# Performance work log

Hardware: AMD Instinct MI355X
Metric: run time of the kernel (lower is better)

The kernel has to match this reference:

```python
import jax, jax.numpy as jnp
import numpy as np

# --- static forest structure: NT complete ternary trees of depth DEPTH ---
BR, DEPTH, NT = 3, 7, 64            # branching factor (=L), edge-levels, num trees
OFF = [(3 ** d - 1) // 2 for d in range(DEPTH + 2)]  # BFS level offsets within a tree
NPT = OFF[DEPTH + 1]                 # nodes per tree = 3280
DIM = NT * NPT                       # total nodes = 209920
C_DIM, NGEN, M_SYM = 8, 8, 128


def build_tree():
    """Returns pos, leaves, batch, roots, levels [(parent_idx, child_idx)], unique-parents per level."""
    base = (np.arange(NT) * NPT)[:, None]
    pos = np.zeros(DIM, dtype=np.int64)
    levels, upar = [], []
    for d in range(1, DEPTH + 1):
        loc = np.arange(OFF[d], OFF[d + 1])
        ch = (base + loc).ravel()                                 # children at depth d (tree-major)
        pa = (base + (OFF[d - 1] + (loc - OFF[d]) // BR)).ravel() # their parents
        pos[ch] = np.tile((loc - OFF[d]) % BR, NT)
        levels.append((pa, ch))
        upar.append((base + np.arange(OFF[d - 1], OFF[d])).ravel())  # unique parents of level d
    leaves = (base + np.arange(OFF[DEPTH], OFF[DEPTH + 1])).ravel()
    batch = np.repeat(np.arange(NT), NPT)
    roots = np.arange(NT) * NPT
    return pos, leaves, batch, roots, levels, upar


def setup_inputs() -> dict:
    key = jax.random.key(0)
    k1, k2, k3, k4, k5 = jax.random.split(key, 5)
    pos_np, leaves_np, batch_np, _, _, _ = build_tree()
    return {
        "lam_A": jax.random.uniform(k1, (C_DIM, C_DIM, BR, NGEN), dtype=jnp.float32),
        "lam_B": jax.random.uniform(k2, (C_DIM, M_SYM, NGEN), dtype=jnp.float32),
        "lam_Pi": jax.random.uniform(k3, (C_DIM, BR, NGEN), dtype=jnp.float32),
        "lam_SP": jax.random.uniform(k4, (BR, NGEN), dtype=jnp.float32),
        "x": jax.random.randint(k5, (DIM,), 0, M_SYM, dtype=jnp.int64),
        "pos": jnp.asarray(pos_np),
        "leaves": jnp.asarray(leaves_np),
        "batch": jnp.asarray(batch_np),
    }


def reference(lam_A, lam_B, lam_Pi, lam_SP, x, pos, leaves, batch):
    # ReversedUpwardDownward (mode='bu') of PosteriorHiddenTreeMarkovModel.
    A = jax.nn.softmax(lam_A, axis=0)   # (C,C,L,G): softmax over first state axis
    Bm = jax.nn.softmax(lam_B, axis=1)  # (C,M,G): softmax over symbols
    Pi = jax.nn.softmax(lam_Pi, axis=0) # (C,L,G)
    SP = jax.nn.softmax(lam_SP, axis=0) # (L,G)
    C, G = A.shape[0], A.shape[-1]
    _, _, _, roots, levels, upar = build_tree()  # static structure

    beta = jnp.zeros((DIM, C, G), lam_A.dtype)
    t_beta = jnp.zeros((DIM, C, G), lam_A.dtype)

    # --- leaves init ---
    Pi_leaves = Pi[:, pos[leaves]]            # (C,Nl,G)
    bl = jnp.transpose(Pi_leaves * Bm[:, x[leaves]], (1, 0, 2))  # (Nl,C,G)
    beta = beta.at[leaves].set(bl / bl.sum(1, keepdims=True))

    # --- upward pass (deepest level first) ---
    for (pa, ch), u in zip(reversed(levels), reversed(upar)):
        SP_ch = SP[pos[ch]][:, None, None, :]                 # (E,1,1,G)
        A_ch = jnp.transpose(A[:, :, pos[ch]], (2, 0, 1, 3))  # (E,C,C,G)
        tb = (SP_ch * A_ch * beta[ch][:, None]).sum(2)        # (E,C,G) sum over child state
        t_beta = t_beta.at[pa].add(tb)
        bu = t_beta[u] * jnp.transpose(Bm[:, x[u]], (1, 0, 2))
        beta = beta.at[u].set(bu / bu.sum(1, keepdims=True))

    # --- downward pass ---
    eps = jnp.zeros((DIM, C, G), lam_A.dtype)
    ell = jnp.zeros((DIM, G), lam_A.dtype)
    eps = eps.at[roots].set(beta[roots])
    for pa, ch in levels:
        SP_ch = SP[pos[ch]]                                   # (E,G)
        A_ch = jnp.transpose(A[:, :, pos[ch]], (2, 0, 1, 3))  # (E,C,C,G)
        trans = SP_ch[:, None, None, :] * A_ch
        ej = (eps[pa][:, :, None, :] * trans * beta[ch][:, None, :, :]
              / t_beta[pa][:, :, None, :])                    # (E,C,C,G) joint posterior
        eps = eps.at[ch].set(ej.sum(1))
        ell = ell.at[ch].add((ej * jnp.log(A_ch)).sum((1, 2))
                             + ej.sum((1, 2)) * jnp.log(SP_ch))
    ell = ell + (eps * jnp.transpose(Bm[:, x], (1, 0, 2))).sum(1)
    ell = ell.at[leaves].add((eps[leaves] * jnp.transpose(jnp.log(Pi_leaves), (1, 0, 2))).sum(1))
    return -jax.ops.segment_sum(ell, batch, num_segments=NT)  # (NT,G)
```

## Files before the change

### kernel.cpp

```cpp
#include <hip/hip_runtime.h>
#include <hip/hip_fp16.h>


namespace {

constexpr int kNPT = 3280;
constexpr int kRS  = 72;
constexpr int kAS  = 68;
constexpr unsigned kMAGIC  = 0x13579BDFu;
constexpr unsigned kMAGIC2 = 0x2468ACEFu;
__device__ __constant__ int LO[6] = {0, 1, 4, 13, 40, 121};
__device__ __constant__ int P3[5] = {1, 3, 9, 27, 81};

#define AGENT_LD(p)    __hip_atomic_load((p), __ATOMIC_RELAXED, __HIP_MEMORY_SCOPE_AGENT)
#define AGENT_ST(p, v) __hip_atomic_store((p), (v), __ATOMIC_RELAXED, __HIP_MEMORY_SCOPE_AGENT)

__device__ __forceinline__ void leaf_beta(const float* __restrict__ sPi,
                                          const float* __restrict__ pBm,
                                          int p, int xv, int g, float* b)
{
    float s = 0.f;
    #pragma unroll
    for (int c = 0; c < 8; ++c) {
        b[c] = sPi[(c * 3 + p) * 8 + g] * pBm[xv * 64 + c * 8 + g];
        s += b[c];
    }
    float ig = __builtin_amdgcn_rcpf(s);
    #pragma unroll
    for (int c = 0; c < 8; ++c) b[c] *= ig;
}

__device__ __forceinline__ void matvec_acc(const float* __restrict__ arow,
                                           const float* __restrict__ bj,
                                           float spg, float* acc)
{
    #pragma unroll
    for (int j = 0; j < 8; ++j) {
        float4 a0 = *(const float4*)(arow + j * 8);
        float4 a1 = *(const float4*)(arow + j * 8 + 4);
        float cjv = spg * bj[j];
        acc[0] = fmaf(a0.x, cjv, acc[0]); acc[1] = fmaf(a0.y, cjv, acc[1]);
        acc[2] = fmaf(a0.z, cjv, acc[2]); acc[3] = fmaf(a0.w, cjv, acc[3]);
        acc[4] = fmaf(a1.x, cjv, acc[4]); acc[5] = fmaf(a1.y, cjv, acc[5]);
        acc[6] = fmaf(a1.z, cjv, acc[6]); acc[7] = fmaf(a1.w, cjv, acc[7]);
    }
}

__global__ __launch_bounds__(256, 2)
void fused(const float* __restrict__ lamA, const float* __restrict__ lamB,
           const float* __restrict__ lamPi, const float* __restrict__ lamSP,
           const int* __restrict__ x, float* __restrict__ out,
           unsigned* __restrict__ sy, float* __restrict__ bmG,
           float* __restrict__ b3, float* __restrict__ e3)
{
    const int tid = threadIdx.x, w = tid >> 6, lane = tid & 63;
    const int n = lane >> 3, g = lane & 7;
    __shared__ __align__(16) float sAg[24 * kAS];
    __shared__ __align__(16) float sLAg[24 * kAS];
    __shared__ float sPi[192], sLPi[192], sSP[24], sLSP[24];
    __shared__ float bW[4][40 * kRS];
    __shared__ __half bMidH[13 * 64];
    __shared__ float sMs[13 * 8];
    __shared__ unsigned char xW[4][124];
    unsigned* trCnt = sy + 32;
    unsigned* trFlg = sy + 2080;

    if (tid == 0) {
        if (blockIdx.x == 0) {
            for (int i = 0; i < 64; ++i) AGENT_ST(&trCnt[i * 32], 0u);
            __builtin_amdgcn_s_waitcnt(0);
            AGENT_ST(&sy[0], kMAGIC);
        }
        unsigned long sp = 0;
        while (AGENT_LD(&sy[0]) != kMAGIC) {
            if (++sp > (1UL << 24)) break;
            __builtin_amdgcn_s_sleep(2);
        }
    }
    __syncthreads();

    if (blockIdx.x == 0) {
        float* rr = &bW[0][0];
        int row = tid >> 2, part = tid & 3;
        int c = row >> 3, gg = row & 7, m0 = part * 32;
        float mx = -1e30f;
        for (int mm = 0; mm < 32; ++mm)
            mx = fmaxf(mx, lamB[(c * 128 + m0 + mm) * 8 + gg]);
        rr[tid] = mx;
        __syncthreads();
        float m4 = fmaxf(fmaxf(rr[row * 4], rr[row * 4 + 1]),
                         fmaxf(rr[row * 4 + 2], rr[row * 4 + 3]));
        float s = 0.f;
        for (int mm = 0; mm < 32; ++mm)
            s += expf(lamB[(c * 128 + m0 + mm) * 8 + gg] - m4);
        rr[256 + tid] = s;
        __syncthreads();
        float stot = rr[256 + row * 4] + rr[256 + row * 4 + 1]
                   + rr[256 + row * 4 + 2] + rr[256 + row * 4 + 3];
        float inv = 1.f / stot;
        for (int mm = 0; mm < 32; ++mm)
            AGENT_ST(&bmG[(m0 + mm) * 64 + c * 8 + gg],
                     expf(lamB[(c * 128 + m0 + mm) * 8 + gg] - m4) * inv);
        __syncthreads();
        if (tid == 0) AGENT_ST(&sy[4], kMAGIC2);
    }
    for (int col = tid; col < 192; col += 256) {
        int j = col / 24; int rem = col - j * 24; int p = rem >> 3; int gg = rem & 7;
        float v[8]; float mx = -1e30f;
        #pragma unroll
        for (int i = 0; i < 8; ++i) {
            v[i] = lamA[((i * 8 + j) * 3 + p) * 8 + gg];
            mx = fmaxf(mx, v[i]);
        }
        float s = 0.f;
        #pragma unroll
        for (int i = 0; i < 8; ++i) { v[i] = expf(v[i] - mx); s += v[i]; }
        float inv = 1.f / s;
        int base = (gg * 3 + p) * kAS + j * 8;
        #pragma unroll
        for (int i = 0; i < 8; ++i) {
            float sm = v[i] * inv;
            sAg[base + i]  = sm;
            sLAg[base + i] = sm * logf(sm);
        }
    }
    for (int col = tid; col < 24; col += 256) {
        int p = col >> 3; int gg = col & 7;
        float v[8]; float mx = -1e30f;
        #pragma unroll
        for (int c = 0; c < 8; ++c) {
            v[c] = lamPi[(c * 3 + p) * 8 + gg];
            mx = fmaxf(mx, v[c]);
        }
        float s = 0.f;
        #pragma unroll
        for (int c = 0; c < 8; ++c) { v[c] = expf(v[c] - mx); s += v[c]; }
        float inv = 1.f / s;
        #pragma unroll
        for (int c = 0; c < 8; ++c) {
            int idx = (c * 3 + p) * 8 + gg;
            float sm = v[c] * inv;
            sPi[idx]  = sm;
            sLPi[idx] = logf(sm);
        }
    }
    if (tid < 8) {
        int gg = tid;
        float v0 = lamSP[gg], v1 = lamSP[8 + gg], v2 = lamSP[16 + gg];
        float mx = fmaxf(v0, fmaxf(v1, v2));
        float e0 = expf(v0 - mx), e1 = expf(v1 - mx), e2 = expf(v2 - mx);
        float inv = 1.f / (e0 + e1 + e2);
        sSP[gg] = e0 * inv; sSP[8 + gg] = e1 * inv; sSP[16 + gg] = e2 * inv;
        sLSP[gg] = logf(e0 * inv); sLSP[8 + gg] = logf(e1 * inv); sLSP[16 + gg] = logf(e2 * inv);
    }
    if (tid == 0) {
        unsigned long sp = 0;
        while (AGENT_LD(&sy[4]) != kMAGIC2) {
            if (++sp > (1UL << 24)) break;
            __builtin_amdgcn_s_sleep(2);
        }
        __threadfence();
    }
    __syncthreads();

    const float* pBm = bmG;
    const int id = blockIdx.x * 4 + w, t = id / 27, q = id % 27, xb = t * kNPT;
    float* bw = &bW[w][0];
    unsigned char* xw = &xW[w][0];

    for (int u = lane; u < 121; u += 64) {
        int gx;
        if (u == 0)       gx = 13 + q;
        else if (u < 4)   gx = 40  + q * 3  + (u - 1);
        else if (u < 13)  gx = 121 + q * 9  + (u - 4);
        else if (u < 40)  gx = 364 + q * 27 + (u - 13);
        else              gx = 1093 + q * 81 + (u - 40);
        xw[u] = (unsigned char)x[xb + gx];
    }
    __builtin_amdgcn_wave_barrier();

    for (int e = 3; e >= 0; --e) {
        int cnt = P3[e];
        for (int base = 0; base < cnt; base += 8) {
            int node = base + n;
            if (node < cnt) {
                float acc[8];
                #pragma unroll
                for (int i = 0; i < 8; ++i) acc[i] = 0.f;
                #pragma unroll
                for (int k = 0; k < 3; ++k) {
                    float bj[8];
                    if (e == 3) {
                        leaf_beta(sPi, pBm, k, xw[40 + 3 * node + k], g, bj);
                    } else {
                        int co = (LO[e + 1] + 3 * node + k) * kRS + g;
                        #pragma unroll
                        for (int j = 0; j < 8; ++j) bj[j] = bw[co + j * 8];
                    }
                    matvec_acc(&sAg[(g * 3 + k) * kAS], bj, sSP[k * 8 + g], acc);
                }
                if (e == 0) {
                    #pragma unroll
                    for (int i = 0; i < 8; ++i) bw[i * 8 + g] = acc[i];
                    int xv = xw[0];
                    float s = 0.f;
                    #pragma unroll
                    for (int i = 0; i < 8; ++i) { acc[i] *= pBm[xv * 64 + i * 8 + g]; s += acc[i]; }
                    float ig = __builtin_amdgcn_rcpf(s);
                    #pragma unroll
                    for (int i = 0; i < 8; ++i)
                        AGENT_ST(&b3[id * 64 + i * 8 + g], acc[i] * ig);
                } else {
                    int slot = LO[e] + node;
                    int xv = xw[slot];
                    float s = 0.f;
                    #pragma unroll
                    for (int i = 0; i < 8; ++i) { acc[i] *= pBm[xv * 64 + i * 8 + g]; s += acc[i]; }
                    float ig = __builtin_amdgcn_rcpf(s);
                    int bo = slot * kRS + g;
                    #pragma unroll
                    for (int i = 0; i < 8; ++i) bw[bo + i * 8] = acc[i] * ig;
                    bw[slot * kRS + 64 + g] = s;
                }
            }
        }
        __builtin_amdgcn_wave_barrier();
    }
    __builtin_amdgcn_s_waitcnt(0);
    if (lane == 0)
        __hip_atomic_fetch_add(&trCnt[t * 32], 1u, __ATOMIC_RELAXED,
                               __HIP_MEMORY_SCOPE_AGENT);

    if (q == 0) {
        unsigned long sp = 0;
        while (AGENT_LD(&trCnt[t * 32]) < 27u) {
            if (++sp > (1UL << 22)) break;
            __builtin_amdgcn_s_sleep(1);
        }
        __threadfence();
        float ellm = 0.f;
        for (int f = 2; f >= 0; --f) {
            int cnt = (f == 2) ? 9 : (f == 1 ? 3 : 1);
            int pl0 = (f == 2) ? 4 : (f == 1 ? 1 : 0);
            int cl0 = (f == 1) ? 4 : 1;
            for (int base = 0; base < cnt; base += 8) {
                int pi = base + n;
                if (pi < cnt) {
                    float acc[8];
                    #pragma unroll
                    for (int i = 0; i < 8; ++i) acc[i] = 0.f;
                    #pragma unroll
                    for (int k = 0; k < 3; ++k) {
                        float bj[8];
                        if (f == 2) {
                            const float* src = b3 + (t * 27 + 3 * pi + k) * 64 + g;
                            #pragma unroll
                            for (int j = 0; j < 8; ++j) bj[j] = src[j * 8];
                        } else {
                            int co = (cl0 + 3 * pi + k) * 64 + g;
                            #pragma unroll
                            for (int j = 0; j < 8; ++j)
                                bj[j] = __half2float(bMidH[co + j * 8]);
                        }
                        matvec_acc(&sAg[(g * 3 + k) * kAS], bj, sSP[k * 8 + g], acc);
                    }
                    int slot = pl0 + pi;
                    int xv = x[xb + slot];
                    float s = 0.f;
                    #pragma unroll
                    for (int i = 0; i < 8; ++i) { acc[i] *= pBm[xv * 64 + i * 8 + g]; s += acc[i]; }
                    float ig = __builtin_amdgcn_rcpf(s);
                    int bo = slot * 64 + g;
                    #pragma unroll
                    for (int i = 0; i < 8; ++i)
                        bMidH[bo + i * 8] = __float2half(acc[i] * ig);
                    sMs[slot * 8 + g] = s;
                }
            }
            __builtin_amdgcn_wave_barrier();
        }
        if (n == 0) {
            int xv = x[xb];
            float invs = __builtin_amdgcn_rcpf(sMs[g]);
            #pragma unroll
            for (int c = 0; c < 8; ++c)
                ellm += __half2float(bMidH[c * 8 + g]) * pBm[xv * 64 + c * 8 + g];
            #pragma unroll
            for (int c = 0; c < 8; ++c)
                bMidH[c * 8 + g] = __float2half(pBm[xv * 64 + c * 8 + g] * invs);
        }
        __builtin_amdgcn_wave_barrier();
        for (int f = 1; f <= 3; ++f) {
            int cnt = (f == 1) ? 3 : (f == 2 ? 9 : 27);
            int cl0 = (f == 1) ? 1 : (f == 2 ? 4 : 13);
            int pl0 = (f == 1) ? 0 : (f == 2 ? 1 : 4);
            for (int base = 0; base < cnt; base += 8) {
                int ci = base + n;
                if (ci < cnt) {
                    int p = ci % 3;
                    int ps = (pl0 + ci / 3) * 64 + g;
                    float r[8];
                    #pragma unroll
                    for (int i = 0; i < 8; ++i) r[i] = __half2float(bMidH[ps + i * 8]);
                    float bj[8]; float sv = 0.f;
                    if (f == 3) {
                        const float* src = b3 + (t * 27 + ci) * 64 + g;
                        #pragma unroll
                        for (int j = 0; j < 8; ++j) bj[j] = src[j * 8];
                    } else {
                        int co = (cl0 + ci) * 64 + g;
                        #pragma unroll
                        for (int j = 0; j < 8; ++j) bj[j] = __half2float(bMidH[co + j * 8]);
                        sv = sMs[(cl0 + ci) * 8 + g];
                    }
                    float spg = sSP[p * 8 + g];
                    const float* arow = &sAg[(g * 3 + p) * kAS];
                    const float* lrow = &sLAg[(g * 3 + p) * kAS];
                    float esum = 0.f, lg = 0.f;
                    float ev[8];
                    #pragma unroll
                    for (int j = 0; j < 8; ++j) {
                        float4 a0 = *(const float4*)(arow + j * 8);
                        float4 a1 = *(const float4*)(arow + j * 8 + 4);
                        float4 l0 = *(const float4*)(lrow + j * 8);
                        float4 l1 = *(const float4*)(lrow + j * 8 + 4);
                        float s1 = r[0] * a0.x; s1 = fmaf(r[1], a0.y, s1);
                        s1 = fmaf(r[2], a0.z, s1); s1 = fmaf(r[3], a0.w, s1);
                        s1 = fmaf(r[4], a1.x, s1); s1 = fmaf(r[5], a1.y, s1);
                        s1 = fmaf(r[6], a1.z, s1); s1 = fmaf(r[7], a1.w, s1);
                        float s2 = r[0] * l0.x; s2 = fmaf(r[1], l0.y, s2);
                        s2 = fmaf(r[2], l0.z, s2); s2 = fmaf(r[3], l0.w, s2);
                        s2 = fmaf(r[4], l1.x, s2); s2 = fmaf(r[5], l1.y, s2);
                        s2 = fmaf(r[6], l1.z, s2); s2 = fmaf(r[7], l1.w, s2);
                        float bs = spg * bj[j];
                        ev[j] = bs * s1;
                        lg    = fmaf(bs, s2, lg);
                        esum += ev[j];
                    }
                    lg = fmaf(esum, sLSP[p * 8 + g], lg);
                    int xv = x[xb + cl0 + ci];
                    float Bmv[8];
                    #pragma unroll
                    for (int c = 0; c < 8; ++c) {
                        Bmv[c] = pBm[xv * 64 + c * 8 + g];
                        lg = fmaf(ev[c], Bmv[c], lg);
                    }
                    if (f == 3) {
                        #pragma unroll
                        for (int j = 0; j < 8; ++j)
                            AGENT_ST(&e3[(t * 27 + ci) * 64 + j * 8 + g], ev[j]);
                    } else {
                        int co = (cl0 + ci) * 64 + g;
                        #pragma unroll
                        for (int j = 0; j < 8; ++j)
                            bMidH[co + j * 8] = __float2half(
                                ev[j] * Bmv[j] * __builtin_amdgcn_rcpf(bj[j] * sv));
                    }
                    ellm += lg;
                }
            }
            __builtin_amdgcn_wave_barrier();
        }
        ellm += __shfl_xor(ellm, 8);
        ellm += __shfl_xor(ellm, 16);
        ellm += __shfl_xor(ellm, 32);
        if (n == 0) atomicAdd(&out[t * 8 + g], -ellm);
        __builtin_amdgcn_s_waitcnt(0);
        if (lane == 0) AGENT_ST(&trFlg[t * 32], kMAGIC2);
    }

    {
        unsigned long sp = 0;
        while (AGENT_LD(&trFlg[t * 32]) != kMAGIC2) {
            if (++sp > (1UL << 22)) break;
            __builtin_amdgcn_s_sleep(1);
        }
    }
    bw[lane] = AGENT_LD(&e3[id * 64 + lane]) * __builtin_amdgcn_rcpf(bw[lane]);
    __builtin_amdgcn_wave_barrier();

    float ell = 0.f;
    for (int e = 1; e <= 4; ++e) {
        int cnt = P3[e], pl0 = LO[e - 1];
        for (int base = 0; base < cnt; base += 8) {
            int ci = base + n;
            if (ci < cnt) {
                int p = ci % 3;
                int ps = (pl0 + ci / 3) * kRS + g;
                float r[8];
                #pragma unroll
                for (int i = 0; i < 8; ++i) r[i] = bw[ps + i * 8];
                float bj[8]; float sv = 0.f;
                int xv;
                if (e == 4) {
                    xv = xw[40 + ci];
                    leaf_beta(sPi, pBm, p, xv, g, bj);
                } else {
                    int slot = LO[e] + ci;
                    xv = xw[slot];
                    int co = slot * kRS + g;
                    #pragma unroll
                    for (int j = 0; j < 8; ++j) bj[j] = bw[co + j * 8];
                    sv = bw[slot * kRS + 64 + g];
                }
                float spg = sSP[p * 8 + g];
                const float* arow = &sAg[(g * 3 + p) * kAS];
                const float* lrow = &sLAg[(g * 3 + p) * kAS];
                float esum = 0.f, lg = 0.f;
                float ev[8];
                #pragma unroll
                for (int j = 0; j < 8; ++j) {
                    float4 a0 = *(const float4*)(arow + j * 8);
                    float4 a1 = *(const float4*)(arow + j * 8 + 4);
                    float4 l0 = *(const float4*)(lrow + j * 8);
                    float4 l1 = *(const float4*)(lrow + j * 8 + 4);
                    float s1 = r[0] * a0.x; s1 = fmaf(r[1], a0.y, s1);
                    s1 = fmaf(r[2], a0.z, s1); s1 = fmaf(r[3], a0.w, s1);
                    s1 = fmaf(r[4], a1.x, s1); s1 = fmaf(r[5], a1.y, s1);
                    s1 = fmaf(r[6], a1.z, s1); s1 = fmaf(r[7], a1.w, s1);
                    float s2 = r[0] * l0.x; s2 = fmaf(r[1], l0.y, s2);
                    s2 = fmaf(r[2], l0.z, s2); s2 = fmaf(r[3], l0.w, s2);
                    s2 = fmaf(r[4], l1.x, s2); s2 = fmaf(r[5], l1.y, s2);
                    s2 = fmaf(r[6], l1.z, s2); s2 = fmaf(r[7], l1.w, s2);
                    float bs = spg * bj[j];
                    ev[j] = bs * s1;
                    lg    = fmaf(bs, s2, lg);
                    esum += ev[j];
                }
                lg = fmaf(esum, sLSP[p * 8 + g], lg);
                float Bmv[8];
                #pragma unroll
                for (int c = 0; c < 8; ++c) {
                    Bmv[c] = pBm[xv * 64 + c * 8 + g];
                    lg = fmaf(ev[c], Bmv[c], lg);
                }
                if (e < 4) {
                    int slot = LO[e] + ci;
                    int co = slot * kRS + g;
                    #pragma unroll
                    for (int j = 0; j < 8; ++j)
                        bw[co + j * 8] = ev[j] * Bmv[j]
                            * __builtin_amdgcn_rcpf(bj[j] * sv);
                } else {
                    #pragma unroll
                    for (int c = 0; c < 8; ++c)
                        lg = fmaf(ev[c], sLPi[(c * 3 + p) * 8 + g], lg);
                }
                ell += lg;
            }
        }
        __builtin_amdgcn_wave_barrier();
    }

    ell += __shfl_xor(ell, 8);
    ell += __shfl_xor(ell, 16);
    ell += __shfl_xor(ell, 32);
    if (n == 0) atomicAdd(&out[t * 8 + g], -ell);
}

}

extern "C" void kernel_launch(void* const* d_in, const int* in_sizes, int n_in,
                              void* d_out, int out_size, void* d_ws, size_t ws_size,
                              hipStream_t stream) {
    const float* lamA  = (const float*)d_in[0];
    const float* lamB  = (const float*)d_in[1];
    const float* lamPi = (const float*)d_in[2];
    const float* lamSP = (const float*)d_in[3];
    const int*   x     = (const int*)d_in[4];
    float* out = (float*)d_out;
    unsigned* sy  = (unsigned*)d_ws;
    float* bmG = (float*)d_ws + 8192;
    float* b3  = bmG + 8192;
    float* e3  = b3 + 1728 * 64;

    fused<<<dim3(432), dim3(256), 0, stream>>>(
        lamA, lamB, lamPi, lamSP, x, out, sy, bmG, b3, e3);
}
```

Baseline: 144.4 us.

## Spread per-tree top-level pass across a full block instead of one wave

Each tree now gets 7 blocks (28 waves, 27 of them active), so the grid grows from 432 to 448 blocks. The last block of each tree runs the top-of-tree upward/downward pass with all four waves, one node per lane group, using __syncthreads between levels. Before, a single wave walked those levels serially. The aim is to shorten this serial critical-path stage. The cost is an extra mostly-idle wave per tree and block-level barriers.

```diff
diff --git a/kernel.cpp b/kernel.cpp
--- a/kernel.cpp
+++ b/kernel.cpp
@@ -164,122 +164,131 @@
     __syncthreads();
 
     const float* pBm = bmG;
-    const int id = blockIdx.x * 4 + w, t = id / 27, q = id % 27, xb = t * kNPT;
+    const int t = blockIdx.x / 7, rb = blockIdx.x - t * 7;
+    const int q = rb * 4 + w;
+    const int id = t * 27 + q;
+    const int xb = t * kNPT;
     float* bw = &bW[w][0];
     unsigned char* xw = &xW[w][0];
 
-    for (int u = lane; u < 121; u += 64) {
-        int gx;
-        if (u == 0)       gx = 13 + q;
-        else if (u < 4)   gx = 40  + q * 3  + (u - 1);
-        else if (u < 13)  gx = 121 + q * 9  + (u - 4);
-        else if (u < 40)  gx = 364 + q * 27 + (u - 13);
-        else              gx = 1093 + q * 81 + (u - 40);
-        xw[u] = (unsigned char)x[xb + gx];
-    }
-    __builtin_amdgcn_wave_barrier();
-
-    for (int e = 3; e >= 0; --e) {
-        int cnt = P3[e];
-        for (int base = 0; base < cnt; base += 8) {
-            int node = base + n;
-            if (node < cnt) {
-                float acc[8];
-                #pragma unroll
-                for (int i = 0; i < 8; ++i) acc[i] = 0.f;
-                #pragma unroll
-                for (int k = 0; k < 3; ++k) {
-                    float bj[8];
-                    if (e == 3) {
-                        leaf_beta(sPi, pBm, k, xw[40 + 3 * node + k], g, bj);
+    if (q < 27) {
+        for (int u = lane; u < 121; u += 64) {
+            int gx;
+            if (u == 0)       gx = 13 + q;
+            else if (u < 4)   gx = 40  + q * 3  + (u - 1);
+            else if (u < 13)  gx = 121 + q * 9  + (u - 4);
+            else if (u < 40)  gx = 364 + q * 27 + (u - 13);
+            else              gx = 1093 + q * 81 + (u - 40);
+            xw[u] = (unsigned char)x[xb + gx];
+        }
+        __builtin_amdgcn_wave_barrier();
+
+        for (int e = 3; e >= 0; --e) {
+            int cnt = P3[e];
+            for (int base = 0; base < cnt; base += 8) {
+                int node = base + n;
+                if (node < cnt) {
+                    float acc[8];
+                    #pragma unroll
+                    for (int i = 0; i < 8; ++i) acc[i] = 0.f;
+                    #pragma unroll
+                    for (int k = 0; k < 3; ++k) {
+                        float bj[8];
+                        if (e == 3) {
+                            leaf_beta(sPi, pBm, k, xw[40 + 3 * node + k], g, bj);
+                        } else {
+                            int co = (LO[e + 1] + 3 * node + k) * kRS + g;
+                            #pragma unroll
+                            for (int j = 0; j < 8; ++j) bj[j] = bw[co + j * 8];
+                        }
+                        matvec_acc(&sAg[(g * 3 + k) * kAS], bj, sSP[k * 8 + g], acc);
+                    }
+                    if (e == 0) {
+                        #pragma unroll
+                        for (int i = 0; i < 8; ++i) bw[i * 8 + g] = acc[i];
+                        int xv = xw[0];
+                        float s = 0.f;
+                        #pragma unroll
+                        for (int i = 0; i < 8; ++i) { acc[i] *= pBm[xv * 64 + i * 8 + g]; s += acc[i]; }
+                        float ig = __builtin_amdgcn_rcpf(s);
+                        #pragma unroll
+                        for (int i = 0; i < 8; ++i)
+                            AGENT_ST(&b3[id * 64 + i * 8 + g], acc[i] * ig);
                     } else {
-                        int co = (LO[e + 1] + 3 * node + k) * kRS + g;
-                        #pragma unroll
-                        for (int j = 0; j < 8; ++j) bj[j] = bw[co + j * 8];
+                        int slot = LO[e] + node;
+                        int xv = xw[slot];
+                        float s = 0.f;
+                        #pragma unroll
+                        for (int i = 0; i < 8; ++i) { acc[i] *= pBm[xv * 64 + i * 8 + g]; s += acc[i]; }
+                        float ig = __builtin_amdgcn_rcpf(s);
+                        int bo = slot * kRS + g;
+                        #pragma unroll
+                        for (int i = 0; i < 8; ++i) bw[bo + i * 8] = acc[i] * ig;
+                        bw[slot * kRS + 64 + g] = s;
                     }
-                    matvec_acc(&sAg[(g * 3 + k) * kAS], bj, sSP[k * 8 + g], acc);
-                }
-                if (e == 0) {
-                    #pragma unroll
-                    for (int i = 0; i < 8; ++i) bw[i * 8 + g] = acc[i];
-                    int xv = xw[0];
-                    float s = 0.f;
-                    #pragma unroll
-                    for (int i = 0; i < 8; ++i) { acc[i] *= pBm[xv * 64 + i * 8 + g]; s += acc[i]; }
-                    float ig = __builtin_amdgcn_rcpf(s);
-                    #pragma unroll
-                    for (int i = 0; i < 8; ++i)
-                        AGENT_ST(&b3[id * 64 + i * 8 + g], acc[i] * ig);
-                } else {
-                    int slot = LO[e] + node;
-                    int xv = xw[slot];
-                    float s = 0.f;
-                    #pragma unroll
-                    for (int i = 0; i < 8; ++i) { acc[i] *= pBm[xv * 64 + i * 8 + g]; s += acc[i]; }
-                    float ig = __builtin_amdgcn_rcpf(s);
-                    int bo = slot * kRS + g;
-                    #pragma unroll
-                    for (int i = 0; i < 8; ++i) bw[bo + i * 8] = acc[i] * ig;
-                    bw[slot * kRS + 64 + g] = s;
                 }
             }
-        }
-        __builtin_amdgcn_wave_barrier();
-    }
-    __builtin_amdgcn_s_waitcnt(0);
-    if (lane == 0)
-        __hip_atomic_fetch_add(&trCnt[t * 32], 1u, __ATOMIC_RELAXED,
-                               __HIP_MEMORY_SCOPE_AGENT);
-
-    if (q == 0) {
-        unsigned long sp = 0;
-        while (AGENT_LD(&trCnt[t * 32]) < 27u) {
-            if (++sp > (1UL << 22)) break;
-            __builtin_amdgcn_s_sleep(1);
+            __builtin_amdgcn_wave_barrier();
+        }
+        __builtin_amdgcn_s_waitcnt(0);
+        if (lane == 0)
+            __hip_atomic_fetch_add(&trCnt[t * 32], 1u, __ATOMIC_RELAXED,
+                                   __HIP_MEMORY_SCOPE_AGENT);
+    }
+
+    if (rb == 6) {
+        {
+            unsigned long sp = 0;
+            while (AGENT_LD(&trCnt[t * 32]) < 27u) {
+                if (++sp > (1UL << 22)) break;
+                __builtin_amdgcn_s_sleep(1);
+            }
         }
         __threadfence();
+        __syncthreads();
+
         float ellm = 0.f;
+        const int vn = (w << 3) + n;
+
         for (int f = 2; f >= 0; --f) {
             int cnt = (f == 2) ? 9 : (f == 1 ? 3 : 1);
             int pl0 = (f == 2) ? 4 : (f == 1 ? 1 : 0);
             int cl0 = (f == 1) ? 4 : 1;
-            for (int base = 0; base < cnt; base += 8) {
-                int pi = base + n;
-                if (pi < cnt) {
-                    float acc[8];
-                    #pragma unroll
-                    for (int i = 0; i < 8; ++i) acc[i] = 0.f;
-                    #pragma unroll
-                    for (int k = 0; k < 3; ++k) {
-                        float bj[8];
-                        if (f == 2) {
-                            const float* src = b3 + (t * 27 + 3 * pi + k) * 64 + g;
-                            #pragma unroll
-                            for (int j = 0; j < 8; ++j) bj[j] = src[j * 8];
-                        } else {
-                            int co = (cl0 + 3 * pi + k) * 64 + g;
-                            #pragma unroll
-                            for (int j = 0; j < 8; ++j)
-                                bj[j] = __half2float(bMidH[co + j * 8]);
-                        }
-                        matvec_acc(&sAg[(g * 3 + k) * kAS], bj, sSP[k * 8 + g], acc);
+            int pi = vn;
+            if (pi < cnt) {
+                float acc[8];
+                #pragma unroll
+                for (int i = 0; i < 8; ++i) acc[i] = 0.f;
+                #pragma unroll
+                for (int k = 0; k < 3; ++k) {
+                    float bj[8];
+                    if (f == 2) {
+                        const float* src = b3 + (t * 27 + 3 * pi + k) * 64 + g;
+                        #pragma unroll
+                        for (int j = 0; j < 8; ++j) bj[j] = src[j * 8];
+                    } else {
+                        int co = (cl0 + 3 * pi + k) * 64 + g;
+                        #pragma unroll
+                        for (int j = 0; j < 8; ++j)
+                            bj[j] = __half2float(bMidH[co + j * 8]);
                     }
-                    int slot = pl0 + pi;
-                    int xv = x[xb + slot];
-                    float s = 0.f;
-                    #pragma unroll
-                    for (int i = 0; i < 8; ++i) { acc[i] *= pBm[xv * 64 + i * 8 + g]; s += acc[i]; }
-                    float ig = __builtin_amdgcn_rcpf(s);
-                    int bo = slot * 64 + g;
-                    #pragma unroll
-                    for (int i = 0; i < 8; ++i)
-                        bMidH[bo + i * 8] = __float2half(acc[i] * ig);
-                    sMs[slot * 8 + g] = s;
-                }
+                    matvec_acc(&sAg[(g * 3 + k) * kAS], bj, sSP[k * 8 + g], acc);
+                }
+                int slot = pl0 + pi;
+                int xv = x[xb + slot];
+                float s = 0.f;
+                #pragma unroll
+                for (int i = 0; i < 8; ++i) { acc[i] *= pBm[xv * 64 + i * 8 + g]; s += acc[i]; }
+                float ig = __builtin_amdgcn_rcpf(s);
+                int bo = slot * 64 + g;
+                #pragma unroll
+                for (int i = 0; i < 8; ++i)
+                    bMidH[bo + i * 8] = __float2half(acc[i] * ig);
+                sMs[slot * 8 + g] = s;
             }
-            __builtin_amdgcn_wave_barrier();
-        }
-        if (n == 0) {
+            __syncthreads();
+        }
+        if (w == 0 && n == 0) {
             int xv = x[xb];
             float invs = __builtin_amdgcn_rcpf(sMs[g]);
             #pragma unroll
@@ -289,119 +298,28 @@
             for (int c = 0; c < 8; ++c)
                 bMidH[c * 8 + g] = __float2half(pBm[xv * 64 + c * 8 + g] * invs);
         }
-        __builtin_amdgcn_wave_barrier();
+        __syncthreads();
         for (int f = 1; f <= 3; ++f) {
             int cnt = (f == 1) ? 3 : (f == 2 ? 9 : 27);
             int cl0 = (f == 1) ? 1 : (f == 2 ? 4 : 13);
             int pl0 = (f == 1) ? 0 : (f == 2 ? 1 : 4);
-            for (int base = 0; base < cnt; base += 8) {
-                int ci = base + n;
-                if (ci < cnt) {
-                    int p = ci % 3;
-                    int ps = (pl0 + ci / 3) * 64 + g;
-                    float r[8];
-                    #pragma unroll
-                    for (int i = 0; i < 8; ++i) r[i] = __half2float(bMidH[ps + i * 8]);
-                    float bj[8]; float sv = 0.f;
-                    if (f == 3) {
-                        const float* src = b3 + (t * 27 + ci) * 64 + g;
-                        #pragma unroll
-                        for (int j = 0; j < 8; ++j) bj[j] = src[j * 8];
-                    } else {
-                        int co = (cl0 + ci) * 64 + g;
-                        #pragma unroll
-                        for (int j = 0; j < 8; ++j) bj[j] = __half2float(bMidH[co + j * 8]);
-                        sv = sMs[(cl0 + ci) * 8 + g];
-                    }
-                    float spg = sSP[p * 8 + g];
-                    const float* arow = &sAg[(g * 3 + p) * kAS];
-                    const float* lrow = &sLAg[(g * 3 + p) * kAS];
-                    float esum = 0.f, lg = 0.f;
-                    float ev[8];
-                    #pragma unroll
-                    for (int j = 0; j < 8; ++j) {
-                        float4 a0 = *(const float4*)(arow + j * 8);
-                        float4 a1 = *(const float4*)(arow + j * 8 + 4);
-                        float4 l0 = *(const float4*)(lrow + j * 8);
-                        float4 l1 = *(const float4*)(lrow + j * 8 + 4);
-                        float s1 = r[0] * a0.x; s1 = fmaf(r[1], a0.y, s1);
-                        s1 = fmaf(r[2], a0.z, s1); s1 = fmaf(r[3], a0.w, s1);
-                        s1 = fmaf(r[4], a1.x, s1); s1 = fmaf(r[5], a1.y, s1);
-                        s1 = fmaf(r[6], a1.z, s1); s1 = fmaf(r[7], a1.w, s1);
-                        float s2 = r[0] * l0.x; s2 = fmaf(r[1], l0.y, s2);
-                        s2 = fmaf(r[2], l0.z, s2); s2 = fmaf(r[3], l0.w, s2);
-                        s2 = fmaf(r[4], l1.x, s2); s2 = fmaf(r[5], l1.y, s2);
-                        s2 = fmaf(r[6], l1.z, s2); s2 = fmaf(r[7], l1.w, s2);
-                        float bs = spg * bj[j];
-                        ev[j] = bs * s1;
-                        lg    = fmaf(bs, s2, lg);
-                        esum += ev[j];
-                    }
-                    lg = fmaf(esum, sLSP[p * 8 + g], lg);
-                    int xv = x[xb + cl0 + ci];
-                    float Bmv[8];
-                    #pragma unroll
-                    for (int c = 0; c < 8; ++c) {
-                        Bmv[c] = pBm[xv * 64 + c * 8 + g];
-                        lg = fmaf(ev[c], Bmv[c], lg);
-                    }
-                    if (f == 3) {
-                        #pragma unroll
-                        for (int j = 0; j < 8; ++j)
-                            AGENT_ST(&e3[(t * 27 + ci) * 64 + j * 8 + g], ev[j]);
-                    } else {
-                        int co = (cl0 + ci) * 64 + g;
-                        #pragma unroll
-                        for (int j = 0; j < 8; ++j)
-                            bMidH[co + j * 8] = __float2half(
-                                ev[j] * Bmv[j] * __builtin_amdgcn_rcpf(bj[j] * sv));
-                    }
-                    ellm += lg;
-                }
-            }
-            __builtin_amdgcn_wave_barrier();
-        }
-        ellm += __shfl_xor(ellm, 8);
-        ellm += __shfl_xor(ellm, 16);
-        ellm += __shfl_xor(ellm, 32);
-        if (n == 0) atomicAdd(&out[t * 8 + g], -ellm);
-        __builtin_amdgcn_s_waitcnt(0);
-        if (lane == 0) AGENT_ST(&trFlg[t * 32], kMAGIC2);
-    }
-
-    {
-        unsigned long sp = 0;
-        while (AGENT_LD(&trFlg[t * 32]) != kMAGIC2) {
-            if (++sp > (1UL << 22)) break;
-            __builtin_amdgcn_s_sleep(1);
-        }
-    }
-    bw[lane] = AGENT_LD(&e3[id * 64 + lane]) * __builtin_amdgcn_rcpf(bw[lane]);
-    __builtin_amdgcn_wave_barrier();
-
-    float ell = 0.f;
-    for (int e = 1; e <= 4; ++e) {
-        int cnt = P3[e], pl0 = LO[e - 1];
-        for (int base = 0; base < cnt; base += 8) {
-            int ci = base + n;
+            int ci = vn;
             if (ci < cnt) {
                 int p = ci % 3;
-                int ps = (pl0 + ci / 3) * kRS + g;
+                int ps = (pl0 + ci / 3) * 64 + g;
                 float r[8];
                 #pragma unroll
-                for (int i = 0; i < 8; ++i) r[i] = bw[ps + i * 8];
+                for (int i = 0; i < 8; ++i) r[i] = __half2float(bMidH[ps + i * 8]);
                 float bj[8]; float sv = 0.f;
-                int xv;
-                if (e == 4) {
-                    xv = xw[40 + ci];
-                    leaf_beta(sPi, pBm, p, xv, g, bj);
+                if (f == 3) {
+                    const float* src = b3 + (t * 27 + ci) * 64 + g;
+                    #pragma unroll
+                    for (int j = 0; j < 8; ++j) bj[j] = src[j * 8];
                 } else {
-                    int slot = LO[e] + ci;
-                    xv = xw[slot];
-                    int co = slot * kRS + g;
-                    #pragma unroll
-                    for (int j = 0; j < 8; ++j) bj[j] = bw[co + j * 8];
-                    sv = bw[slot * kRS + 64 + g];
+                    int co = (cl0 + ci) * 64 + g;
+                    #pragma unroll
+                    for (int j = 0; j < 8; ++j) bj[j] = __half2float(bMidH[co + j * 8]);
+                    sv = sMs[(cl0 + ci) * 8 + g];
                 }
                 float spg = sSP[p * 8 + g];
                 const float* arow = &sAg[(g * 3 + p) * kAS];
@@ -428,6 +346,96 @@
                     esum += ev[j];
                 }
                 lg = fmaf(esum, sLSP[p * 8 + g], lg);
+                int xv = x[xb + cl0 + ci];
+                float Bmv[8];
+                #pragma unroll
+                for (int c = 0; c < 8; ++c) {
+                    Bmv[c] = pBm[xv * 64 + c * 8 + g];
+                    lg = fmaf(ev[c], Bmv[c], lg);
+                }
+                if (f == 3) {
+                    #pragma unroll
+                    for (int j = 0; j < 8; ++j)
+                        AGENT_ST(&e3[(t * 27 + ci) * 64 + j * 8 + g], ev[j]);
+                } else {
+                    int co = (cl0 + ci) * 64 + g;
+                    #pragma unroll
+                    for (int j = 0; j < 8; ++j)
+                        bMidH[co + j * 8] = __float2half(
+                            ev[j] * Bmv[j] * __builtin_amdgcn_rcpf(bj[j] * sv));
+                }
+                ellm += lg;
+            }
+            __syncthreads();
+        }
+        ellm += __shfl_xor(ellm, 8);
+        ellm += __shfl_xor(ellm, 16);
+        ellm += __shfl_xor(ellm, 32);
+        if (n == 0) atomicAdd(&out[t * 8 + g], -ellm);
+        __builtin_amdgcn_s_waitcnt(0);
+        __syncthreads();
+        if (tid == 0) AGENT_ST(&trFlg[t * 32], kMAGIC2);
+        if (q == 27) return;
+    } else {
+        unsigned long sp = 0;
+        while (AGENT_LD(&trFlg[t * 32]) != kMAGIC2) {
+            if (++sp > (1UL << 22)) break;
+            __builtin_amdgcn_s_sleep(1);
+        }
+    }
+
+    bw[lane] = AGENT_LD(&e3[id * 64 + lane]) * __builtin_amdgcn_rcpf(bw[lane]);
+    __builtin_amdgcn_wave_barrier();
+
+    float ell = 0.f;
+    for (int e = 1; e <= 4; ++e) {
+        int cnt = P3[e], pl0 = LO[e - 1];
+        for (int base = 0; base < cnt; base += 8) {
+            int ci = base + n;
+            if (ci < cnt) {
+                int p = ci % 3;
+                int ps = (pl0 + ci / 3) * kRS + g;
+                float r[8];
+                #pragma unroll
+                for (int i = 0; i < 8; ++i) r[i] = bw[ps + i * 8];
+                float bj[8]; float sv = 0.f;
+                int xv;
+                if (e == 4) {
+                    xv = xw[40 + ci];
+                    leaf_beta(sPi, pBm, p, xv, g, bj);
+                } else {
+                    int slot = LO[e] + ci;
+                    xv = xw[slot];
+                    int co = slot * kRS + g;
+                    #pragma unroll
+                    for (int j = 0; j < 8; ++j) bj[j] = bw[co + j * 8];
+                    sv = bw[slot * kRS + 64 + g];
+                }
+                float spg = sSP[p * 8 + g];
+                const float* arow = &sAg[(g * 3 + p) * kAS];
+                const float* lrow = &sLAg[(g * 3 + p) * kAS];
+                float esum = 0.f, lg = 0.f;
+                float ev[8];
+                #pragma unroll
+                for (int j = 0; j < 8; ++j) {
+                    float4 a0 = *(const float4*)(arow + j * 8);
+                    float4 a1 = *(const float4*)(arow + j * 8 + 4);
+                    float4 l0 = *(const float4*)(lrow + j * 8);
+                    float4 l1 = *(const float4*)(lrow + j * 8 + 4);
+                    float s1 = r[0] * a0.x; s1 = fmaf(r[1], a0.y, s1);
+                    s1 = fmaf(r[2], a0.z, s1); s1 = fmaf(r[3], a0.w, s1);
+                    s1 = fmaf(r[4], a1.x, s1); s1 = fmaf(r[5], a1.y, s1);
+                    s1 = fmaf(r[6], a1.z, s1); s1 = fmaf(r[7], a1.w, s1);
+                    float s2 = r[0] * l0.x; s2 = fmaf(r[1], l0.y, s2);
+                    s2 = fmaf(r[2], l0.z, s2); s2 = fmaf(r[3], l0.w, s2);
+                    s2 = fmaf(r[4], l1.x, s2); s2 = fmaf(r[5], l1.y, s2);
+                    s2 = fmaf(r[6], l1.z, s2); s2 = fmaf(r[7], l1.w, s2);
+                    float bs = spg * bj[j];
+                    ev[j] = bs * s1;
+                    lg    = fmaf(bs, s2, lg);
+                    esum += ev[j];
+                }
+                lg = fmaf(esum, sLSP[p * 8 + g], lg);
                 float Bmv[8];
                 #pragma unroll
                 for (int c = 0; c < 8; ++c) {
@@ -474,6 +482,6 @@
     float* b3  = bmG + 8192;
     float* e3  = b3 + 1728 * 64;
 
-    fused<<<dim3(432), dim3(256), 0, stream>>>(
+    fused<<<dim3(448), dim3(256), 0, stream>>>(
         lamA, lamB, lamPi, lamSP, x, out, sy, bmG, b3, e3);
 }
```

New measurement: 142.4 us (median of 2 runs). No clear change (-1.4%).
